# Kernel tuning notes

Measured on AMD Instinct MI355X. Metric: run time of the kernel, lower is better.

Reference implementation:

```python
import jax, jax.numpy as jnp
import numpy as np
from jax import lax

EPS = 1e-5
K = 3            # FreqFilter kernel size
G = 8            # groups = out_ch // channel_per_group = 64 // 8


def conv2d(x, w, pad):
    return lax.conv_general_dilated(
        x, w, window_strides=(1, 1), padding=[(pad, pad), (pad, pad)],
        dimension_numbers=("NCHW", "OIHW", "NCHW"))


def leaky(x):
    return jnp.where(x >= 0, x, 0.01 * x)


def freq_filter(y, wf, gamma, beta):
    # y: (n, c, h, w) with c = 64
    n, c, h, w = y.shape
    yp = jnp.pad(y, ((0, 0), (0, 0), (1, 1), (1, 1)), mode="reflect")
    sig = conv2d(yp, wf, pad=0)                       # (n, G*K*K, h, w)
    # BatchNorm2d in training mode: batch statistics over (N,H,W)
    mu = sig.mean(axis=(0, 2, 3), keepdims=True)
    var = sig.var(axis=(0, 2, 3), keepdims=True)
    sig = (sig - mu) * lax.rsqrt(var + EPS)
    sig = sig * gamma[None, :, None, None] + beta[None, :, None, None]
    sig = jax.nn.softmax(sig, axis=1)                 # softmax over all G*K*K channels
    sig = sig.reshape(n, G, K * K, h, w)              # channel = g*(K*K) + k
    # kernel = identity (delta at center tap) - sigma
    center = K * K // 2
    delta = jnp.zeros((K * K,), sig.dtype).at[center].set(1.0)
    kernel = delta[None, None, :, None, None] - sig   # (n, G, 9, h, w)
    # im2col patches of the reflect-padded input, unfold ordering (row-major taps)
    patches = jnp.stack(
        [yp[:, :, i:i + h, j:j + w] for i in range(K) for j in range(K)],
        axis=2)                                        # (n, c, 9, h, w)
    patches = patches.reshape(n, G, c // G, K * K, h, w)
    out = jnp.einsum("ngckhw,ngkhw->ngchw", patches, kernel)
    return out.reshape(n, c, h, w)


def hin(x):
    # InstanceNorm2d (affine=False) on first half of channels
    half = x.shape[1] // 2
    a = x[:, :half]
    mu = a.mean(axis=(2, 3), keepdims=True)
    var = a.var(axis=(2, 3), keepdims=True)
    a = (a - mu) * lax.rsqrt(var + EPS)
    return jnp.concatenate([a, x[:, half:]], axis=1)


def setup_inputs() -> dict:
    key = jax.random.key(0)
    ks = jax.random.split(key, 8)
    n, cin, cout, h, w = 4, 64, 64, 256, 256
    return {
        "x": jax.random.normal(ks[0], (n, cin, h, w), jnp.float32),
        "w1": jax.random.normal(ks[1], (cout, cin, 3, 3), jnp.float32) * 0.05,
        "b1": jax.random.normal(ks[2], (cout,), jnp.float32) * 0.01,
        "wf": jax.random.normal(ks[3], (G * K * K, cout, 3, 3), jnp.float32) * 0.06,
        "bn_gamma": jnp.ones((G * K * K,), jnp.float32),
        "bn_beta": jnp.zeros((G * K * K,), jnp.float32),
        "w2": jax.random.normal(ks[4], (cout, cout, 3, 3), jnp.float32) * 0.05,
        "b2": jax.random.normal(ks[5], (cout,), jnp.float32) * 0.01,
        "wr": jax.random.normal(ks[6], (cout, cin, 1, 1), jnp.float32) * 0.1,
        "br": jax.random.normal(ks[7], (cout,), jnp.float32) * 0.01,
    }


def reference(x, w1, b1, wf, bn_gamma, bn_beta, w2, b2, wr, br):
    y = conv2d(x, w1, pad=1) + b1[None, :, None, None]
    y = freq_filter(y, wf, bn_gamma, bn_beta)
    y = leaky(hin(y))
    y = leaky(conv2d(y, w2, pad=1) + b2[None, :, None, None])
    res = conv2d(x, wr, pad=0) + br[None, :, None, None]
    return res + y
```

## Files before the change

### kernel.cpp

```cpp
#include <hip/hip_runtime.h>

typedef unsigned short u16;
typedef __attribute__((ext_vector_type(8))) short bf16x8;
typedef __attribute__((ext_vector_type(16))) float f32x16;
typedef __attribute__((address_space(3))) void lds_void;
typedef __attribute__((address_space(1))) const void gbl_void;

#define NN 4
#define HH 256
#define WW 256
#define PD 258
#define CIN 64
#define EPSV 1e-5f

__device__ __forceinline__ float b2f(u16 x){ union{unsigned u; float f;} q; q.u = ((unsigned)x)<<16; return q.f; }
__device__ __forceinline__ u16 f2b(float f){ union{float f; unsigned u;} q; q.f = f; unsigned r = q.u + 0x7FFF + ((q.u>>16)&1u); return (u16)(r>>16); }
__device__ __forceinline__ float leakyf(float x){ return x >= 0.f ? x : 0.01f*x; }

__global__ void prep_kernel(const float* __restrict__ w1, const float* __restrict__ wf,
                            const float* __restrict__ w2, const float* __restrict__ wr,
                            u16* __restrict__ wB1, u16* __restrict__ wBf,
                            u16* __restrict__ wB2, u16* __restrict__ wBr){
  int idx = blockIdx.x*256 + threadIdx.x;
  if (idx < 36864){
    int e = idx & 7, lane = (idx >> 3) & 63, rest = idx >> 9;
    int tap = rest % 9, rest2 = rest / 9;
    int cg = rest2 & 1, kq = rest2 >> 1;
    int cout = cg*32 + (lane & 31);
    int cin  = kq*16 + (lane >> 5)*8 + e;
    int src = (cout*64 + cin)*9 + tap;
    wB1[idx] = f2b(w1[src]);
    wB2[idx] = f2b(w2[src]);
  }
  if (idx < 55296){
    int e = idx & 7, lane = (idx >> 3) & 63, rest = idx >> 9;
    int tap = rest % 9, rest2 = rest / 9;
    int cg = rest2 % 3, kq = rest2 / 3;
    int cout = cg*32 + (lane & 31);
    int cin  = kq*16 + (lane >> 5)*8 + e;
    float v = (cout < 72) ? wf[(cout*64 + cin)*9 + tap] : 0.f;
    wBf[idx] = f2b(v);
  }
  if (idx < 4096){
    int e = idx & 7, lane = (idx >> 3) & 63, rest = idx >> 9;
    int cg = rest & 1, kq = rest >> 1;
    int cout = cg*32 + (lane & 31);
    int cin  = kq*16 + (lane >> 5)*8 + e;
    wBr[idx] = f2b(wr[cout*64 + cin]);
  }
}

__global__ __launch_bounds__(256) void padx_kernel(const float* __restrict__ x, u16* __restrict__ xpad){
  int n = blockIdx.x >> 8, h = blockIdx.x & 255, t = threadIdx.x;
  u16* dstrow = xpad + ((size_t)(n*PD + h + 1)*PD)*CIN;
  const uint4 z = {0,0,0,0};
  #pragma unroll
  for (int c8 = 0; c8 < 8; ++c8){
    u16 buf[8];
    #pragma unroll
    for (int j = 0; j < 8; ++j)
      buf[j] = f2b(x[((size_t)(n*64 + c8*8 + j))*65536 + h*256 + t]);
    *(uint4*)(dstrow + (size_t)(t+1)*CIN + c8*8) = *(uint4*)buf;
  }
  if (t == 0)   { for (int c8 = 0; c8 < 8; ++c8) *(uint4*)(dstrow + 0*CIN   + c8*8) = z; }
  if (t == 255) { for (int c8 = 0; c8 < 8; ++c8) *(uint4*)(dstrow + 257*CIN + c8*8) = z; }
  if (h == 0 || h == 255){
    u16* brow = xpad + ((size_t)(n*PD + (h == 0 ? 0 : 257))*PD)*CIN;
    for (int p = t; p < PD; p += 256)
      for (int c8 = 0; c8 < 8; ++c8) *(uint4*)(brow + (size_t)p*CIN + c8*8) = z;
  }
}

__global__ void reflect_kernel(u16* __restrict__ y1pad){
  int idx = blockIdx.x*256 + threadIdx.x;
  if (idx >= 4*1028*8) return;
  int n = idx/(1028*8), rem = idx%(1028*8), p = rem >> 3, cc = rem & 7;
  int pr, pc;
  if      (p < 258)  { pr = 0;   pc = p; }
  else if (p < 516)  { pr = 257; pc = p - 258; }
  else if (p < 772)  { pr = 1 + (p - 516); pc = 0; }
  else               { pr = 1 + (p - 772); pc = 257; }
  int sr = (pr == 0) ? 2 : ((pr == 257) ? 255 : pr);
  int sc = (pc == 0) ? 2 : ((pc == 257) ? 255 : pc);
  uint4 v = *(const uint4*)(y1pad + ((size_t)(n*PD + sr)*PD + sc)*CIN + cc*8);
  *(uint4*)(y1pad + ((size_t)(n*PD + pr)*PD + pc)*CIN + cc*8) = v;
}

template<int NCG, int MODE>
__global__ __launch_bounds__(NCG*128, 4) void conv_mfma(
    const u16* __restrict__ Ain, const u16* __restrict__ wB, const float* __restrict__ bias,
    u16* __restrict__ outB, float* __restrict__ outF,
    const u16* __restrict__ xpad, const u16* __restrict__ wBr,
    const float* __restrict__ br,
    float* __restrict__ bnsum, float* __restrict__ bnsumsq,
    const float* __restrict__ hmu, const float* __restrict__ hrs){

  constexpr int NC  = (MODE == 1) ? 72 : 64;
  constexpr int NCP = NC + 8;
  constexpr int TPB = NCG*128;
  constexpr int RND = (2112 + TPB - 1)/TPB;
  __shared__ __align__(16) char smem[2112*16];
  __shared__ float hmr[64];

  int t = threadIdx.x, lane = t & 63, wv = t >> 6;
  int l31 = lane & 31, l1 = lane >> 5;
  int cg = wv % NCG, ph = wv / NCG;
  int bid = blockIdx.x;
  int sb = (bid & 7)*256 + (bid >> 3);
  int n = sb >> 9, rem = sb & 511, rowb = rem >> 2, colb = rem & 3;
  int h0 = rowb*2, w0 = colb*64;

  if (MODE == 2 && t < 64) hmr[t] = (t < 32) ? hmu[n*32 + t] : hrs[n*32 + (t - 32)];

  {
    const u16* base = Ain + ((size_t)(n*PD + h0)*PD + w0)*CIN;
    #pragma unroll
    for (int rnd = 0; rnd < RND; ++rnd){
      int c = rnd*TPB + t;
      if (c < 2112){
        int row = c / 528, rem2 = c - row*528;
        int px = rem2 >> 3, sub = rem2 & 7;
        int subs = sub ^ (px & 7);
        const u16* src = base + (size_t)row*PD*CIN + (size_t)(px*8 + subs)*8;
        __builtin_amdgcn_global_load_lds((gbl_void*)src,
                                         (lds_void*)(smem + (size_t)c*16), 16, 0, 0);
      }
    }
  }
  __syncthreads();

  if (MODE == 2){
    #pragma unroll
    for (int rnd = 0; rnd < RND; ++rnd){
      int c = rnd*TPB + t;
      if (c < 2112){
        int row = c / 528, rem2 = c - row*528;
        int px = rem2 >> 3, sub = rem2 & 7;
        int gpr = h0 + row, gpc = w0 + px;
        uint4* p = (uint4*)(smem + (size_t)c*16);
        if (gpr == 0 || gpr == 257 || gpc == 0 || gpc == 257){
          uint4 z = {0,0,0,0}; *p = z;
        } else {
          int cg8 = sub ^ (px & 7);
          uint4 v = *p;
          u16* e = (u16*)&v;
          if (cg8 < 4){
            #pragma unroll
            for (int j = 0; j < 8; ++j){
              float f = (b2f(e[j]) - hmr[cg8*8 + j]) * hmr[32 + cg8*8 + j];
              e[j] = f2b(leakyf(f));
            }
          } else {
            #pragma unroll
            for (int j = 0; j < 8; ++j) e[j] = f2b(leakyf(b2f(e[j])));
          }
          *p = v;
        }
      }
    }
    __syncthreads();
  }

  f32x16 acc[2];
  #pragma unroll
  for (int pg = 0; pg < 2; ++pg)
    #pragma unroll
    for (int i = 0; i < 16; ++i) acc[pg][i] = 0.f;

  #pragma unroll
  for (int kq = 0; kq < 4; ++kq){
    bf16x8 wfr[9];
    #pragma unroll
    for (int tap = 0; tap < 9; ++tap)
      wfr[tap] = *(const bf16x8*)(wB + ((size_t)((kq*NCG + cg)*9 + tap)*64 + lane)*8);
    #pragma unroll
    for (int pg = 0; pg < 2; ++pg){
      #pragma unroll
      for (int tap = 0; tap < 9; ++tap){
        int wrow = ph + tap/3;
        int wcol = pg*32 + l31 + tap%3;
        int chunk = (kq*2 + l1) ^ (wcol & 7);
        bf16x8 afr = *(const bf16x8*)(smem + ((((wrow*66 + wcol) << 3) + chunk) << 4));
        acc[pg] = __builtin_amdgcn_mfma_f32_32x32x16_bf16(afr, wfr[tap], acc[pg], 0, 0, 0);
      }
    }
  }

  int cout = cg*32 + l31;

  if (MODE < 2){
    __syncthreads();
    u16* Bx = (u16*)smem;
    float* bnpart = (float*)(smem + 24576);
    if (MODE == 1){
      float s = 0.f, q = 0.f;
      #pragma unroll
      for (int pg = 0; pg < 2; ++pg)
        #pragma unroll
        for (int reg = 0; reg < 16; ++reg){ float v = acc[pg][reg]; s += v; q += v*v; }
      s += __shfl_xor(s, 32); q += __shfl_xor(q, 32);
      if (l1 == 0){ bnpart[(wv*32 + l31)*2 + 0] = s; bnpart[(wv*32 + l31)*2 + 1] = q; }
    }
    #pragma unroll
    for (int pg = 0; pg < 2; ++pg){
      float bv = (MODE == 0) ? bias[cout] : 0.f;
      #pragma unroll
      for (int reg = 0; reg < 16; ++reg){
        int rowD = (reg & 3) + 8*(reg >> 2) + 4*l1;
        int p = ph*64 + pg*32 + rowD;
        if (MODE == 0 || cout < 72)
          Bx[p*NCP + cout] = f2b(acc[pg][reg] + bv);
      }
    }
    __syncthreads();
    constexpr int nch = NC/8;
    for (int idx = t; idx < 128*nch; idx += TPB){
      int px = idx/nch, c8 = idx - px*nch;
      int rr = px >> 6, cc = px & 63;
      uint4 v = *(const uint4*)(Bx + px*NCP + c8*8);
      if (MODE == 0)
        *(uint4*)(outB + ((size_t)(n*PD + h0 + 1 + rr)*PD + (w0 + 1 + cc))*CIN + c8*8) = v;
      else
        *(uint4*)(outB + ((size_t)(n*65536 + (h0 + rr)*256 + w0 + cc))*72 + c8*8) = v;
    }
    if (MODE == 1 && t < 192){
      int c = t >> 1, which = t & 1;
      if (c < 72){
        int cgf = c >> 5, ci = c & 31;
        float v = bnpart[((cgf*32) + ci)*2 + which] + bnpart[(((NCG + cgf)*32) + ci)*2 + which];
        atomicAdd(which ? &bnsumsq[c] : &bnsum[c], v);
      }
    }
  } else {
    f32x16 racc[2];
    #pragma unroll
    for (int pg = 0; pg < 2; ++pg)
      #pragma unroll
      for (int i = 0; i < 16; ++i) racc[pg][i] = 0.f;
    const u16* Xrow = xpad + ((size_t)(n*PD + h0 + 1 + ph)*PD + (w0 + 1))*CIN;
    #pragma unroll
    for (int kq = 0; kq < 4; ++kq){
      bf16x8 wr8 = *(const bf16x8*)(wBr + ((size_t)((kq*2 + cg)*64 + lane))*8);
      #pragma unroll
      for (int pg = 0; pg < 2; ++pg){
        bf16x8 xfr = *(const bf16x8*)(Xrow + (size_t)(pg*32 + l31)*CIN + kq*16 + l1*8);
        racc[pg] = __builtin_amdgcn_mfma_f32_32x32x16_bf16(xfr, wr8, racc[pg], 0, 0, 0);
      }
    }
    float bv = bias[cout], bb = br[cout];
    float* orow = outF + ((size_t)(n*64 + cout))*65536 + (h0 + ph)*256 + w0;
    #pragma unroll
    for (int pg = 0; pg < 2; ++pg){
      #pragma unroll
      for (int q = 0; q < 4; ++q){
        float4 o;
        o.x = leakyf(acc[pg][q*4+0] + bv) + racc[pg][q*4+0] + bb;
        o.y = leakyf(acc[pg][q*4+1] + bv) + racc[pg][q*4+1] + bb;
        o.z = leakyf(acc[pg][q*4+2] + bv) + racc[pg][q*4+2] + bb;
        o.w = leakyf(acc[pg][q*4+3] + bv) + racc[pg][q*4+3] + bb;
        int px = pg*32 + 8*q + 4*l1;
        *(float4*)(orow + px) = o;
      }
    }
  }
}

__global__ void bnfinal_kernel(const float* __restrict__ bnsum, const float* __restrict__ bnsumsq,
                               const float* __restrict__ gamma, const float* __restrict__ beta,
                               float* __restrict__ bnscale, float* __restrict__ bnshift){
  int c = threadIdx.x;
  if (c < 72){
    const float M = 262144.f;
    float mu  = bnsum[c] / M;
    float var = bnsumsq[c] / M - mu*mu;
    float sc  = gamma[c] * rsqrtf(var + EPSV);
    bnscale[c] = sc;
    bnshift[c] = beta[c] - mu*sc;
  }
}

__global__ __launch_bounds__(256, 4) void filter_kernel(const u16* __restrict__ sig,
                                                        const u16* __restrict__ y1pad,
                                                        const float* __restrict__ bnscale,
                                                        const float* __restrict__ bnshift,
                                                        u16* __restrict__ y2pad,
                                                        float* __restrict__ hinsum,
                                                        float* __restrict__ hinsumsq){
  __shared__ __align__(16) char smem[2112*16];
  __shared__ float sc[72], sh[72];

  int t = threadIdx.x, lane = t & 63, wv = t >> 6;
  if (t < 72){ sc[t] = bnscale[t]; sh[t] = bnshift[t]; }
  int bid = blockIdx.x;
  int sb = (bid & 7)*256 + (bid >> 3);
  int n = sb >> 9, rem = sb & 511, rowb = rem >> 2, colb = rem & 3;
  int h0 = rowb*2, w0 = colb*64;
  int p = t & 127, r = p >> 6, c = p & 63, half = t >> 7;

  {
    const u16* base = y1pad + ((size_t)(n*PD + h0)*PD + w0)*CIN;
    #pragma unroll
    for (int rnd = 0; rnd < 9; ++rnd){
      if (rnd < 8 || wv == 0){
        int cch = rnd*256 + wv*64 + lane;
        int row = cch / 528, rem2 = cch - row*528;
        int px = rem2 >> 3, sub = rem2 & 7;
        int subs = sub ^ (px & 7);
        const u16* src = base + (size_t)row*PD*CIN + (size_t)(px*8 + subs)*8;
        __builtin_amdgcn_global_load_lds((gbl_void*)src,
                                         (lds_void*)(smem + (rnd*256 + wv*64)*16), 16, 0, 0);
      }
    }
  }

  float sv[72];
  const u16* sp = sig + ((size_t)(n*65536 + (h0 + r)*256 + w0 + c))*72;
  #pragma unroll
  for (int i = 0; i < 9; ++i){
    uint4 v = *(const uint4*)(sp + i*8);
    const u16* e = (const u16*)&v;
    #pragma unroll
    for (int j = 0; j < 8; ++j) sv[i*8+j] = b2f(e[j]);
  }
  __syncthreads();
  float mx = -1e30f;
  #pragma unroll
  for (int cc = 0; cc < 72; ++cc){ sv[cc] = sv[cc]*sc[cc] + sh[cc]; mx = fmaxf(mx, sv[cc]); }
  float sum = 0.f;
  #pragma unroll
  for (int cc = 0; cc < 72; ++cc){ sv[cc] = __expf(sv[cc] - mx); sum += sv[cc]; }
  float inv = -1.f/sum;
  float kv[36];
  if (half == 0){
    #pragma unroll
    for (int j = 0; j < 36; ++j) kv[j] = sv[j]*inv;
  } else {
    #pragma unroll
    for (int j = 0; j < 36; ++j) kv[j] = sv[36 + j]*inv;
  }
  #pragma unroll
  for (int c8 = 0; c8 < 4; ++c8) kv[c8*9 + 4] += 1.f;

  float o[32];
  #pragma unroll
  for (int cc = 0; cc < 32; ++cc) o[cc] = 0.f;
  #pragma unroll
  for (int i = 0; i < 3; ++i){
    #pragma unroll
    for (int j = 0; j < 3; ++j){
      int wcol = c + j, wrow = r + i;
      #pragma unroll
      for (int c8 = 0; c8 < 4; ++c8){
        int chunk = half*4 + c8;
        uint4 v = *(const uint4*)(smem + ((((wrow*66 + wcol) << 3) + (chunk ^ (wcol & 7))) << 4));
        const u16* e = (const u16*)&v;
        float k = kv[c8*9 + i*3 + j];
        #pragma unroll
        for (int jj = 0; jj < 8; ++jj) o[c8*8 + jj] = fmaf(k, b2f(e[jj]), o[c8*8 + jj]);
      }
    }
  }
  __syncthreads();

  u16* obuf = (u16*)smem;
  float* ps = (float*)(smem + 20480);
  #pragma unroll
  for (int c8 = 0; c8 < 4; ++c8){
    u16 ob[8];
    #pragma unroll
    for (int jj = 0; jj < 8; ++jj) ob[jj] = f2b(o[c8*8 + jj]);
    *(uint4*)(obuf + p*66 + (half*4 + c8)*8) = *(uint4*)ob;
  }
  __syncthreads();

  {
    int cch = t & 31, seg = t >> 5;
    float s = 0.f, q = 0.f;
    #pragma unroll
    for (int rr = 0; rr < 16; ++rr){
      float v = b2f(obuf[(seg*16 + rr)*66 + cch]);
      s += v; q += v*v;
    }
    ps[(seg*32 + cch)*2 + 0] = s; ps[(seg*32 + cch)*2 + 1] = q;
  }
  for (int idx = t; idx < 1024; idx += 256){
    int pp = idx >> 3, j = idx & 7;
    int rr = pp >> 6, cc = pp & 63;
    uint4 v = *(const uint4*)(obuf + pp*66 + j*8);
    *(uint4*)(y2pad + ((size_t)(n*PD + h0 + 1 + rr)*PD + (w0 + 1 + cc))*CIN + j*8) = v;
  }
  __syncthreads();
  if (t < 64){
    int cc = t >> 1, which = t & 1;
    float v = 0.f;
    #pragma unroll
    for (int seg = 0; seg < 8; ++seg) v += ps[(seg*32 + cc)*2 + which];
    atomicAdd(which ? &hinsumsq[n*32 + cc] : &hinsum[n*32 + cc], v);
  }
}

__global__ void hinfinal_kernel(const float* __restrict__ hinsum, const float* __restrict__ hinsumsq,
                                float* __restrict__ hmu, float* __restrict__ hrs){
  int i = threadIdx.x;
  if (i < 128){
    const float M = 65536.f;
    float mu  = hinsum[i] / M;
    float var = hinsumsq[i] / M - mu*mu;
    hmu[i] = mu;
    hrs[i] = rsqrtf(var + EPSV);
  }
}

extern "C" void kernel_launch(void* const* d_in, const int* in_sizes, int n_in,
                              void* d_out, int out_size, void* d_ws, size_t ws_size,
                              hipStream_t stream){
  const float* x     = (const float*)d_in[0];
  const float* w1    = (const float*)d_in[1];
  const float* b1    = (const float*)d_in[2];
  const float* wf    = (const float*)d_in[3];
  const float* gamma = (const float*)d_in[4];
  const float* beta  = (const float*)d_in[5];
  const float* w2    = (const float*)d_in[6];
  const float* b2    = (const float*)d_in[7];
  const float* wr    = (const float*)d_in[8];
  const float* br    = (const float*)d_in[9];

  char* ws = (char*)d_ws;
  const size_t PADB = (size_t)NN*PD*PD*CIN*2;
  u16* xpad  = (u16*)(ws);
  u16* y1pad = (u16*)(ws + PADB);
  u16* y2pad = (u16*)(ws + 2*PADB);
  float* stats = (float*)(ws + 3*PADB);
  float* bnsum   = stats;        float* bnsumsq = stats + 80;
  float* bnscale = stats + 160;  float* bnshift = stats + 240;
  float* hinsum  = stats + 320;  float* hinsumsq= stats + 448;
  float* hmu     = stats + 576;  float* hrs     = stats + 704;
  u16* wB1 = (u16*)(ws + 3*PADB + 4096);
  u16* wBf = wB1 + 36864;
  u16* wB2 = wBf + 55296;
  u16* wBr = wB2 + 36864;

  u16* sig = (u16*)d_out;
  float* out = (float*)d_out;

  hipMemsetAsync(stats, 0, 4096, stream);
  prep_kernel<<<256, 256, 0, stream>>>(w1, wf, w2, wr, wB1, wBf, wB2, wBr);
  padx_kernel<<<NN*HH, 256, 0, stream>>>(x, xpad);
  conv_mfma<2,0><<<2048, 256, 0, stream>>>(xpad, wB1, b1, y1pad, nullptr, nullptr, nullptr, nullptr, nullptr, nullptr, nullptr, nullptr);
  reflect_kernel<<<(4*1028*8 + 255)/256, 256, 0, stream>>>(y1pad);
  conv_mfma<3,1><<<2048, 384, 0, stream>>>(y1pad, wBf, nullptr, sig, nullptr, nullptr, nullptr, nullptr, bnsum, bnsumsq, nullptr, nullptr);
  bnfinal_kernel<<<1, 80, 0, stream>>>(bnsum, bnsumsq, gamma, beta, bnscale, bnshift);
  filter_kernel<<<2048, 256, 0, stream>>>(sig, y1pad, bnscale, bnshift, y2pad, hinsum, hinsumsq);
  hinfinal_kernel<<<1, 128, 0, stream>>>(hinsum, hinsumsq, hmu, hrs);
  conv_mfma<2,2><<<2048, 256, 0, stream>>>(y2pad, wB2, b2, nullptr, out, xpad, wBr, br, nullptr, nullptr, hmu, hrs);
}
```

Baseline: 218.7 us.

## Make conv blocks persistent over row tiles with double-buffered async LDS staging

```diff
diff --git a/kernel.cpp b/kernel.cpp
--- a/kernel.cpp
+++ b/kernel.cpp
@@ -16,6 +16,15 @@
 __device__ __forceinline__ float b2f(u16 x){ union{unsigned u; float f;} q; q.u = ((unsigned)x)<<16; return q.f; }
 __device__ __forceinline__ u16 f2b(float f){ union{float f; unsigned u;} q; q.f = f; unsigned r = q.u + 0x7FFF + ((q.u>>16)&1u); return (u16)(r>>16); }
 __device__ __forceinline__ float leakyf(float x){ return x >= 0.f ? x : 0.01f*x; }
+
+template<int N> __device__ __forceinline__ void waitvm(){
+  asm volatile("s_waitcnt vmcnt(%0) lgkmcnt(0)" :: "n"(N) : "memory");
+  __builtin_amdgcn_sched_barrier(0);
+}
+__device__ __forceinline__ void waitlg(){
+  asm volatile("s_waitcnt lgkmcnt(0)" ::: "memory");
+  __builtin_amdgcn_sched_barrier(0);
+}
 
 __global__ void prep_kernel(const float* __restrict__ w1, const float* __restrict__ wf,
                             const float* __restrict__ w2, const float* __restrict__ wr,
@@ -87,7 +96,7 @@
 }
 
 template<int NCG, int MODE>
-__global__ __launch_bounds__(NCG*128, 4) void conv_mfma(
+__global__ __launch_bounds__(NCG*128, (NCG==3)?6:4) void conv_mfma(
     const u16* __restrict__ Ain, const u16* __restrict__ wB, const float* __restrict__ bias,
     u16* __restrict__ outB, float* __restrict__ outF,
     const u16* __restrict__ xpad, const u16* __restrict__ wBr,
@@ -95,49 +104,63 @@
     float* __restrict__ bnsum, float* __restrict__ bnsumsq,
     const float* __restrict__ hmu, const float* __restrict__ hrs){
 
-  constexpr int NC  = (MODE == 1) ? 72 : 64;
-  constexpr int NCP = NC + 8;
-  constexpr int TPB = NCG*128;
-  constexpr int RND = (2112 + TPB - 1)/TPB;
-  __shared__ __align__(16) char smem[2112*16];
+  constexpr int NC   = (MODE == 1) ? 72 : 64;
+  constexpr int NCP  = NC + 8;
+  constexpr int TPB  = NCG*128;
+  constexpr int RNDU = 2304/TPB;
+  constexpr int SST  = (MODE==0) ? 4 : ((MODE==1) ? 3 : 8);
+  constexpr int BUFB = 2304*16;
+  __shared__ __align__(16) char smem[2*BUFB];
+  __shared__ float bnacc[NCG*2*32*2];
   __shared__ float hmr[64];
 
   int t = threadIdx.x, lane = t & 63, wv = t >> 6;
   int l31 = lane & 31, l1 = lane >> 5;
   int cg = wv % NCG, ph = wv / NCG;
   int bid = blockIdx.x;
-  int sb = (bid & 7)*256 + (bid >> 3);
-  int n = sb >> 9, rem = sb & 511, rowb = rem >> 2, colb = rem & 3;
-  int h0 = rowb*2, w0 = colb*64;
+  int sb = (bid & 7)*64 + (bid >> 3);
+  int n = sb >> 7, rowb = sb & 127;
+  int h0 = rowb*2;
 
   if (MODE == 2 && t < 64) hmr[t] = (t < 32) ? hmu[n*32 + t] : hrs[n*32 + (t - 32)];
 
-  {
-    const u16* base = Ain + ((size_t)(n*PD + h0)*PD + w0)*CIN;
-    #pragma unroll
-    for (int rnd = 0; rnd < RND; ++rnd){
-      int c = rnd*TPB + t;
-      if (c < 2112){
-        int row = c / 528, rem2 = c - row*528;
-        int px = rem2 >> 3, sub = rem2 & 7;
-        int subs = sub ^ (px & 7);
-        const u16* src = base + (size_t)row*PD*CIN + (size_t)(px*8 + subs)*8;
-        __builtin_amdgcn_global_load_lds((gbl_void*)src,
-                                         (lds_void*)(smem + (size_t)c*16), 16, 0, 0);
-      }
-    }
-  }
-  __syncthreads();
-
-  if (MODE == 2){
-    #pragma unroll
-    for (int rnd = 0; rnd < RND; ++rnd){
-      int c = rnd*TPB + t;
-      if (c < 2112){
+  auto STAGE = [&](int tile, char* dbuf){
+    const u16* base = Ain + ((size_t)(n*PD + h0)*PD + (size_t)tile*64)*CIN;
+    #pragma unroll
+    for (int r = 0; r < RNDU; ++r){
+      int c = r*TPB + t;
+      int cc = (c < 2112) ? c : 0;
+      int row = cc / 528, rem2 = cc - row*528;
+      int px = rem2 >> 3, sub = rem2 & 7;
+      int subs = sub ^ (px & 7);
+      const u16* src = base + (size_t)row*PD*CIN + (size_t)(px*8 + subs)*8;
+      __builtin_amdgcn_global_load_lds((gbl_void*)src,
+                                       (lds_void*)(dbuf + (size_t)c*16), 16, 0, 0);
+    }
+  };
+
+  STAGE(0, smem);
+  STAGE(1, smem + BUFB);
+
+  float bs = 0.f, bq = 0.f;
+  int cout = cg*32 + l31;
+
+  #pragma unroll
+  for (int tile = 0; tile < 4; ++tile){
+    char* buf = smem + (tile & 1)*BUFB;
+    const int w0 = tile*64;
+
+    if (tile == 0)      waitvm<RNDU>();
+    else if (tile < 3)  waitvm<SST + RNDU>();
+    else                waitvm<SST>();
+    __builtin_amdgcn_s_barrier();
+
+    if (MODE == 2){
+      for (int c = t; c < 2112; c += TPB){
         int row = c / 528, rem2 = c - row*528;
         int px = rem2 >> 3, sub = rem2 & 7;
         int gpr = h0 + row, gpc = w0 + px;
-        uint4* p = (uint4*)(smem + (size_t)c*16);
+        uint4* p = (uint4*)(buf + (size_t)c*16);
         if (gpr == 0 || gpr == 257 || gpc == 0 || gpc == 257){
           uint4 z = {0,0,0,0}; *p = z;
         } else {
@@ -157,110 +180,117 @@
           *p = v;
         }
       }
-    }
+      waitlg();
+      __builtin_amdgcn_s_barrier();
+    }
+
+    f32x16 acc[2];
+    #pragma unroll
+    for (int pg = 0; pg < 2; ++pg)
+      #pragma unroll
+      for (int i = 0; i < 16; ++i) acc[pg][i] = 0.f;
+
+    #pragma unroll
+    for (int kq = 0; kq < 4; ++kq){
+      bf16x8 wfr[9];
+      #pragma unroll
+      for (int tap = 0; tap < 9; ++tap)
+        wfr[tap] = *(const bf16x8*)(wB + ((size_t)((kq*NCG + cg)*9 + tap)*64 + lane)*8);
+      #pragma unroll
+      for (int pg = 0; pg < 2; ++pg){
+        #pragma unroll
+        for (int tap = 0; tap < 9; ++tap){
+          int wrow = ph + tap/3;
+          int wcol = pg*32 + l31 + tap%3;
+          int chunk = (kq*2 + l1) ^ (wcol & 7);
+          bf16x8 afr = *(const bf16x8*)(buf + ((((wrow*66 + wcol) << 3) + chunk) << 4));
+          acc[pg] = __builtin_amdgcn_mfma_f32_32x32x16_bf16(afr, wfr[tap], acc[pg], 0, 0, 0);
+        }
+      }
+    }
+
+    if (MODE == 1){
+      #pragma unroll
+      for (int pg = 0; pg < 2; ++pg)
+        #pragma unroll
+        for (int reg = 0; reg < 16; ++reg){ float v = acc[pg][reg]; bs += v; bq += v*v; }
+    }
+
+    waitlg();
+    __builtin_amdgcn_s_barrier();
+
+    if (MODE < 2){
+      u16* Bx = (u16*)buf;
+      #pragma unroll
+      for (int pg = 0; pg < 2; ++pg){
+        float bv = (MODE == 0) ? bias[cout] : 0.f;
+        #pragma unroll
+        for (int reg = 0; reg < 16; ++reg){
+          int rowD = (reg & 3) + 8*(reg >> 2) + 4*l1;
+          int p = ph*64 + pg*32 + rowD;
+          if (MODE == 0 || cout < 72)
+            Bx[p*NCP + cout] = f2b(acc[pg][reg] + bv);
+        }
+      }
+      waitlg();
+      __builtin_amdgcn_s_barrier();
+      constexpr int nch = NC/8;
+      for (int idx = t; idx < 128*nch; idx += TPB){
+        int px = idx/nch, c8 = idx - px*nch;
+        int rr = px >> 6, cc = px & 63;
+        uint4 v = *(const uint4*)(Bx + px*NCP + c8*8);
+        if (MODE == 0)
+          *(uint4*)(outB + ((size_t)(n*PD + h0 + 1 + rr)*PD + (w0 + 1 + cc))*CIN + c8*8) = v;
+        else
+          *(uint4*)(outB + ((size_t)(n*65536 + (h0 + rr)*256 + w0 + cc))*72 + c8*8) = v;
+      }
+      waitlg();
+      __builtin_amdgcn_s_barrier();
+      if (tile < 2) STAGE(tile + 2, buf);
+    } else {
+      if (tile < 2) STAGE(tile + 2, buf);
+      f32x16 racc[2];
+      #pragma unroll
+      for (int pg = 0; pg < 2; ++pg)
+        #pragma unroll
+        for (int i = 0; i < 16; ++i) racc[pg][i] = 0.f;
+      const u16* Xrow = xpad + ((size_t)(n*PD + h0 + 1 + ph)*PD + (w0 + 1))*CIN;
+      #pragma unroll
+      for (int kq = 0; kq < 4; ++kq){
+        bf16x8 wr8 = *(const bf16x8*)(wBr + ((size_t)((kq*2 + cg)*64 + lane))*8);
+        #pragma unroll
+        for (int pg = 0; pg < 2; ++pg){
+          bf16x8 xfr = *(const bf16x8*)(Xrow + (size_t)(pg*32 + l31)*CIN + kq*16 + l1*8);
+          racc[pg] = __builtin_amdgcn_mfma_f32_32x32x16_bf16(xfr, wr8, racc[pg], 0, 0, 0);
+        }
+      }
+      float bv = bias[cout], bb = br[cout];
+      float* orow = outF + ((size_t)(n*64 + cout))*65536 + (h0 + ph)*256 + w0;
+      #pragma unroll
+      for (int pg = 0; pg < 2; ++pg){
+        #pragma unroll
+        for (int q = 0; q < 4; ++q){
+          float4 o;
+          o.x = leakyf(acc[pg][q*4+0] + bv) + racc[pg][q*4+0] + bb;
+          o.y = leakyf(acc[pg][q*4+1] + bv) + racc[pg][q*4+1] + bb;
+          o.z = leakyf(acc[pg][q*4+2] + bv) + racc[pg][q*4+2] + bb;
+          o.w = leakyf(acc[pg][q*4+3] + bv) + racc[pg][q*4+3] + bb;
+          int px = pg*32 + 8*q + 4*l1;
+          *(float4*)(orow + px) = o;
+        }
+      }
+    }
+  }
+
+  if (MODE == 1){
+    bs += __shfl_xor(bs, 32); bq += __shfl_xor(bq, 32);
+    if (l1 == 0){ bnacc[(wv*32 + l31)*2 + 0] = bs; bnacc[(wv*32 + l31)*2 + 1] = bq; }
     __syncthreads();
-  }
-
-  f32x16 acc[2];
-  #pragma unroll
-  for (int pg = 0; pg < 2; ++pg)
-    #pragma unroll
-    for (int i = 0; i < 16; ++i) acc[pg][i] = 0.f;
-
-  #pragma unroll
-  for (int kq = 0; kq < 4; ++kq){
-    bf16x8 wfr[9];
-    #pragma unroll
-    for (int tap = 0; tap < 9; ++tap)
-      wfr[tap] = *(const bf16x8*)(wB + ((size_t)((kq*NCG + cg)*9 + tap)*64 + lane)*8);
-    #pragma unroll
-    for (int pg = 0; pg < 2; ++pg){
-      #pragma unroll
-      for (int tap = 0; tap < 9; ++tap){
-        int wrow = ph + tap/3;
-        int wcol = pg*32 + l31 + tap%3;
-        int chunk = (kq*2 + l1) ^ (wcol & 7);
-        bf16x8 afr = *(const bf16x8*)(smem + ((((wrow*66 + wcol) << 3) + chunk) << 4));
-        acc[pg] = __builtin_amdgcn_mfma_f32_32x32x16_bf16(afr, wfr[tap], acc[pg], 0, 0, 0);
-      }
-    }
-  }
-
-  int cout = cg*32 + l31;
-
-  if (MODE < 2){
-    __syncthreads();
-    u16* Bx = (u16*)smem;
-    float* bnpart = (float*)(smem + 24576);
-    if (MODE == 1){
-      float s = 0.f, q = 0.f;
-      #pragma unroll
-      for (int pg = 0; pg < 2; ++pg)
-        #pragma unroll
-        for (int reg = 0; reg < 16; ++reg){ float v = acc[pg][reg]; s += v; q += v*v; }
-      s += __shfl_xor(s, 32); q += __shfl_xor(q, 32);
-      if (l1 == 0){ bnpart[(wv*32 + l31)*2 + 0] = s; bnpart[(wv*32 + l31)*2 + 1] = q; }
-    }
-    #pragma unroll
-    for (int pg = 0; pg < 2; ++pg){
-      float bv = (MODE == 0) ? bias[cout] : 0.f;
-      #pragma unroll
-      for (int reg = 0; reg < 16; ++reg){
-        int rowD = (reg & 3) + 8*(reg >> 2) + 4*l1;
-        int p = ph*64 + pg*32 + rowD;
-        if (MODE == 0 || cout < 72)
-          Bx[p*NCP + cout] = f2b(acc[pg][reg] + bv);
-      }
-    }
-    __syncthreads();
-    constexpr int nch = NC/8;
-    for (int idx = t; idx < 128*nch; idx += TPB){
-      int px = idx/nch, c8 = idx - px*nch;
-      int rr = px >> 6, cc = px & 63;
-      uint4 v = *(const uint4*)(Bx + px*NCP + c8*8);
-      if (MODE == 0)
-        *(uint4*)(outB + ((size_t)(n*PD + h0 + 1 + rr)*PD + (w0 + 1 + cc))*CIN + c8*8) = v;
-      else
-        *(uint4*)(outB + ((size_t)(n*65536 + (h0 + rr)*256 + w0 + cc))*72 + c8*8) = v;
-    }
-    if (MODE == 1 && t < 192){
+    if (t < 144){
       int c = t >> 1, which = t & 1;
-      if (c < 72){
-        int cgf = c >> 5, ci = c & 31;
-        float v = bnpart[((cgf*32) + ci)*2 + which] + bnpart[(((NCG + cgf)*32) + ci)*2 + which];
-        atomicAdd(which ? &bnsumsq[c] : &bnsum[c], v);
-      }
-    }
-  } else {
-    f32x16 racc[2];
-    #pragma unroll
-    for (int pg = 0; pg < 2; ++pg)
-      #pragma unroll
-      for (int i = 0; i < 16; ++i) racc[pg][i] = 0.f;
-    const u16* Xrow = xpad + ((size_t)(n*PD + h0 + 1 + ph)*PD + (w0 + 1))*CIN;
-    #pragma unroll
-    for (int kq = 0; kq < 4; ++kq){
-      bf16x8 wr8 = *(const bf16x8*)(wBr + ((size_t)((kq*2 + cg)*64 + lane))*8);
-      #pragma unroll
-      for (int pg = 0; pg < 2; ++pg){
-        bf16x8 xfr = *(const bf16x8*)(Xrow + (size_t)(pg*32 + l31)*CIN + kq*16 + l1*8);
-        racc[pg] = __builtin_amdgcn_mfma_f32_32x32x16_bf16(xfr, wr8, racc[pg], 0, 0, 0);
-      }
-    }
-    float bv = bias[cout], bb = br[cout];
-    float* orow = outF + ((size_t)(n*64 + cout))*65536 + (h0 + ph)*256 + w0;
-    #pragma unroll
-    for (int pg = 0; pg < 2; ++pg){
-      #pragma unroll
-      for (int q = 0; q < 4; ++q){
-        float4 o;
-        o.x = leakyf(acc[pg][q*4+0] + bv) + racc[pg][q*4+0] + bb;
-        o.y = leakyf(acc[pg][q*4+1] + bv) + racc[pg][q*4+1] + bb;
-        o.z = leakyf(acc[pg][q*4+2] + bv) + racc[pg][q*4+2] + bb;
-        o.w = leakyf(acc[pg][q*4+3] + bv) + racc[pg][q*4+3] + bb;
-        int px = pg*32 + 8*q + 4*l1;
-        *(float4*)(orow + px) = o;
-      }
+      int cgf = c >> 5, ci = c & 31;
+      float v = bnacc[(cgf*32 + ci)*2 + which] + bnacc[((NCG + cgf)*32 + ci)*2 + which];
+      atomicAdd(which ? &bnsumsq[c] : &bnsum[c], v);
     }
   }
 }
@@ -446,11 +476,11 @@
   hipMemsetAsync(stats, 0, 4096, stream);
   prep_kernel<<<256, 256, 0, stream>>>(w1, wf, w2, wr, wB1, wBf, wB2, wBr);
   padx_kernel<<<NN*HH, 256, 0, stream>>>(x, xpad);
-  conv_mfma<2,0><<<2048, 256, 0, stream>>>(xpad, wB1, b1, y1pad, nullptr, nullptr, nullptr, nullptr, nullptr, nullptr, nullptr, nullptr);
+  conv_mfma<2,0><<<512, 256, 0, stream>>>(xpad, wB1, b1, y1pad, nullptr, nullptr, nullptr, nullptr, nullptr, nullptr, nullptr, nullptr);
   reflect_kernel<<<(4*1028*8 + 255)/256, 256, 0, stream>>>(y1pad);
-  conv_mfma<3,1><<<2048, 384, 0, stream>>>(y1pad, wBf, nullptr, sig, nullptr, nullptr, nullptr, nullptr, bnsum, bnsumsq, nullptr, nullptr);
+  conv_mfma<3,1><<<512, 384, 0, stream>>>(y1pad, wBf, nullptr, sig, nullptr, nullptr, nullptr, nullptr, bnsum, bnsumsq, nullptr, nullptr);
   bnfinal_kernel<<<1, 80, 0, stream>>>(bnsum, bnsumsq, gamma, beta, bnscale, bnshift);
   filter_kernel<<<2048, 256, 0, stream>>>(sig, y1pad, bnscale, bnshift, y2pad, hinsum, hinsumsq);
   hinfinal_kernel<<<1, 128, 0, stream>>>(hinsum, hinsumsq, hmu, hrs);
-  conv_mfma<2,2><<<2048, 256, 0, stream>>>(y2pad, wB2, b2, nullptr, out, xpad, wBr, br, nullptr, nullptr, hmu, hrs);
-}
+  conv_mfma<2,2><<<512, 256, 0, stream>>>(y2pad, wB2, b2, nullptr, out, xpad, wBr, br, nullptr, nullptr, hmu, hrs);
+}
```

New measurement: 277.2 us. 26.7% more time.
